# Kernel optimization log

Hardware: AMD Instinct MI355X
Metric: run time of the kernel (lower is better)

## Reference

```python
import jax, jax.numpy as jnp
import numpy as np

DIM = 768
D_STATE = 64
D_CONV = 4
EXPAND = 2
D_INNER = EXPAND * DIM          # 1536
DT_RANK = (DIM + 15) // 16      # 48
BATCH = 2
SEQ = 1024
EPS = 1e-5


def setup_inputs() -> dict:
    key = jax.random.key(0)
    ks = jax.random.split(key, 10)
    s = 0.02
    x = jax.random.normal(ks[0], (BATCH, SEQ, DIM), dtype=jnp.float32)
    gamma = jnp.ones((DIM,), jnp.float32)
    beta = jnp.zeros((DIM,), jnp.float32)
    W_in = jax.random.normal(ks[1], (2 * D_INNER, DIM), jnp.float32) * s
    conv_w = jax.random.normal(ks[2], (D_INNER, D_CONV), jnp.float32) * s
    conv_b = jnp.zeros((D_INNER,), jnp.float32)
    W_x = jax.random.normal(ks[3], (DT_RANK + 2 * D_STATE, D_INNER), jnp.float32) * s
    W_dt = jax.random.normal(ks[4], (D_INNER, DT_RANK), jnp.float32) * s
    b_dt = jax.random.uniform(ks[5], (D_INNER,), jnp.float32, -4.0, -2.0)  # dt bias ~ log-space init
    # S4D-real init: A_log[d, n] = log(n+1)
    A_log = jnp.log(jnp.broadcast_to(jnp.arange(1, D_STATE + 1, dtype=jnp.float32), (D_INNER, D_STATE)))
    D = jnp.ones((D_INNER,), jnp.float32)
    W_out = jax.random.normal(ks[6], (DIM, D_INNER), jnp.float32) * s
    return {"x": x, "gamma": gamma, "beta": beta, "W_in": W_in,
            "conv_w": conv_w, "conv_b": conv_b, "W_x": W_x,
            "W_dt": W_dt, "b_dt": b_dt, "A_log": A_log, "D": D, "W_out": W_out}


def _silu(v):
    return v * jax.nn.sigmoid(v)


def _mamba_forward(x, gamma, beta, W_in, conv_w, conv_b, W_x, W_dt, b_dt, A_log, D, W_out):
    B, L, _ = x.shape
    # LayerNorm
    mu = jnp.mean(x, axis=-1, keepdims=True)
    var = jnp.mean(jnp.square(x - mu), axis=-1, keepdims=True)
    xn = (x - mu) * jax.lax.rsqrt(var + EPS) * gamma + beta
    # in_proj -> (u, z)
    xz = jnp.einsum('bld,ed->ble', xn, W_in)          # [B, L, 2*D_INNER]
    u, z = jnp.split(xz, 2, axis=-1)                  # each [B, L, D_INNER]
    # depthwise causal conv1d along L
    uc = jnp.transpose(u, (0, 2, 1))                  # [B, C, L]
    uc = jnp.pad(uc, ((0, 0), (0, 0), (D_CONV - 1, 0)))
    kern = conv_w[:, None, :]                         # [C, 1, K]
    uc = jax.lax.conv_general_dilated(
        uc, kern, window_strides=(1,), padding='VALID',
        feature_group_count=D_INNER,
        dimension_numbers=('NCH', 'OIH', 'NCH'))
    uc = uc + conv_b[None, :, None]
    u = _silu(jnp.transpose(uc, (0, 2, 1)))           # [B, L, D_INNER]
    # x_proj -> (dt, Bssm, Cssm)
    x_dbl = jnp.einsum('blc,ec->ble', u, W_x)
    dt = x_dbl[..., :DT_RANK]
    Bssm = x_dbl[..., DT_RANK:DT_RANK + D_STATE]      # [B, L, N]
    Cssm = x_dbl[..., DT_RANK + D_STATE:]             # [B, L, N]
    delta = jax.nn.softplus(jnp.einsum('blr,cr->blc', dt, W_dt) + b_dt)  # [B, L, C]
    A = -jnp.exp(A_log)                               # [C, N]

    # selective scan, time-major
    d_t = jnp.transpose(delta, (1, 0, 2))             # [L, B, C]
    B_t = jnp.transpose(Bssm, (1, 0, 2))              # [L, B, N]
    C_t = jnp.transpose(Cssm, (1, 0, 2))              # [L, B, N]
    u_t = jnp.transpose(u, (1, 0, 2))                 # [L, B, C]

    def step(h, inp):
        d, b, c, uu = inp
        dA = jnp.exp(d[..., None] * A)                # [B, C, N]
        h = dA * h + d[..., None] * b[:, None, :] * uu[..., None]
        y = jnp.sum(h * c[:, None, :], axis=-1) + D * uu
        return h, y

    h0 = jnp.zeros((B, D_INNER, D_STATE), x.dtype)
    _, ys = jax.lax.scan(step, h0, (d_t, B_t, C_t, u_t))
    y = jnp.transpose(ys, (1, 0, 2))                  # [B, L, C]
    y = y * _silu(z)
    return jnp.einsum('blc,dc->bld', y, W_out)


def reference(x, gamma, beta, W_in, conv_w, conv_b, W_x, W_dt, b_dt, A_log, D, W_out):
    return _mamba_forward(x, gamma, beta, W_in, conv_w, conv_b, W_x,
                          W_dt, b_dt, A_log, D, W_out)
```

## Files before the change

kernel.cpp:

```cpp
#include <hip/hip_runtime.h>
#include <math.h>

#define DIMD 768
#define DSTATE 64
#define DINNER 1536
#define DTRANK 48
#define BATCH 2
#define SEQL 1024
#define NTOK (BATCH*SEQL)
#define XDBL_P 192
#define EPSV 1e-5f

typedef __attribute__((ext_vector_type(8))) short bf16x8;
typedef __attribute__((ext_vector_type(4))) float f32x4;

__device__ inline short f2bf(float f) {
  unsigned u = __float_as_uint(f);
  u = u + 0x7FFFu + ((u >> 16) & 1u);
  return (short)(u >> 16);
}

__global__ __launch_bounds__(256) void ln_kernel(const float* __restrict__ x,
                                                 const float* __restrict__ gamma,
                                                 const float* __restrict__ beta,
                                                 short* __restrict__ xnq) {
  int wave = threadIdx.x >> 6;
  int lane = threadIdx.x & 63;
  int row = blockIdx.x * 4 + wave;
  if (row >= NTOK) return;
  const float* xr = x + (size_t)row * DIMD;
  float v[12];
  float s = 0.f, ss = 0.f;
#pragma unroll
  for (int i = 0; i < 12; ++i) {
    v[i] = xr[lane + i*64];
    s += v[i];
    ss += v[i]*v[i];
  }
#pragma unroll
  for (int m = 1; m < 64; m <<= 1) {
    s  += __shfl_xor(s, m);
    ss += __shfl_xor(ss, m);
  }
  float mu   = s * (1.f/DIMD);
  float var  = ss * (1.f/DIMD) - mu*mu;
  float rstd = rsqrtf(var + EPSV);
  short* o = xnq + (size_t)row * DIMD;
#pragma unroll
  for (int i = 0; i < 12; ++i) {
    int j = lane + i*64;
    o[j] = f2bf((v[i] - mu) * rstd * gamma[j] + beta[j]);
  }
}

#define NW_IN  (3072*768)
#define NW_OUT (768*1536)
#define NW_XP  (192*1536)
__global__ __launch_bounds__(256) void cvt_weights_kernel(const float* __restrict__ Win,
                                                          const float* __restrict__ Wout,
                                                          const float* __restrict__ Wx,
                                                          short* __restrict__ qin,
                                                          short* __restrict__ qout,
                                                          short* __restrict__ qx) {
  int idx = blockIdx.x * 256 + threadIdx.x;
  if (idx < NW_IN) { qin[idx] = f2bf(Win[idx]); return; }
  idx -= NW_IN;
  if (idx < NW_OUT) { qout[idx] = f2bf(Wout[idx]); return; }
  idx -= NW_OUT;
  if (idx < NW_XP) {
    int r = idx / 1536;
    qx[idx] = (r < 176) ? f2bf(Wx[idx]) : (short)0;
  }
}

template<int BN>
__global__ __launch_bounds__(256) void gemm_mfma(const short* __restrict__ A,
                                                 const short* __restrict__ B,
                                                 float* __restrict__ C, int ldc, int K) {
  constexpr int BM = 128, BK = 64;
  constexpr int WN = (BN == 128) ? 2 : 1;
  constexpr int WM = 4 / WN;
  constexpr int MFR = BM / (WM * 16);
  constexpr int NFR = BN / (WN * 16);
  constexpr int BSW = (BN * BK * 2) / 4096;
  __shared__ short As[BM * BK];
  __shared__ short Bs[BN * BK];
  const int tid  = threadIdx.x;
  const int wave = tid >> 6, lane = tid & 63;
  const int m0 = blockIdx.y * BM;
  const int n0 = blockIdx.x * BN;
  const int wm = wave / WN, wn = wave % WN;

  const short* aSrc = A + (size_t)(m0 + (tid >> 3)) * K + (tid & 7) * 8;
  const short* bSrc = B + (size_t)(n0 + (tid >> 3)) * K + (tid & 7) * 8;

  f32x4 acc[MFR][NFR];
#pragma unroll
  for (int i = 0; i < MFR; ++i)
#pragma unroll
    for (int j = 0; j < NFR; ++j)
      acc[i][j] = (f32x4){0.f, 0.f, 0.f, 0.f};

  for (int k0 = 0; k0 < K; k0 += BK) {
#pragma unroll
    for (int s = 0; s < 4; ++s)
      __builtin_amdgcn_global_load_lds(
        (const __attribute__((address_space(1))) void*)(aSrc + (size_t)s*32*K + k0),
        (__attribute__((address_space(3))) void*)((char*)As + s*4096 + wave*1024),
        16, 0, 0);
#pragma unroll
    for (int s = 0; s < BSW; ++s)
      __builtin_amdgcn_global_load_lds(
        (const __attribute__((address_space(1))) void*)(bSrc + (size_t)s*32*K + k0),
        (__attribute__((address_space(3))) void*)((char*)Bs + s*4096 + wave*1024),
        16, 0, 0);
    __syncthreads();

#pragma unroll
    for (int kk = 0; kk < 2; ++kk) {
      bf16x8 af[MFR], bfr[NFR];
#pragma unroll
      for (int i = 0; i < MFR; ++i) {
        int r = wm * (BM / WM) + i * 16 + (lane & 15);
        af[i] = *(const bf16x8*)&As[r * BK + kk * 32 + (lane >> 4) * 8];
      }
#pragma unroll
      for (int j = 0; j < NFR; ++j) {
        int r = wn * (BN / WN) + j * 16 + (lane & 15);
        bfr[j] = *(const bf16x8*)&Bs[r * BK + kk * 32 + (lane >> 4) * 8];
      }
#pragma unroll
      for (int i = 0; i < MFR; ++i)
#pragma unroll
        for (int j = 0; j < NFR; ++j)
          acc[i][j] = __builtin_amdgcn_mfma_f32_16x16x32_bf16(af[i], bfr[j], acc[i][j], 0, 0, 0);
    }
    __syncthreads();
  }

  const int cn = lane & 15, cr4 = (lane >> 4) * 4;
#pragma unroll
  for (int i = 0; i < MFR; ++i)
#pragma unroll
    for (int j = 0; j < NFR; ++j)
#pragma unroll
      for (int r = 0; r < 4; ++r) {
        int m = m0 + wm * (BM / WM) + i * 16 + cr4 + r;
        int n = n0 + wn * (BN / WN) + j * 16 + cn;
        C[(size_t)m * ldc + n] = acc[i][j][r];
      }
}

template<int ACT>
__global__ __launch_bounds__(256) void gemm_nt(const float* __restrict__ A, int lda,
                                               const float* __restrict__ W, int ldw,
                                               const float* __restrict__ bias,
                                               float* __restrict__ C, int ldc,
                                               int M, int N, int K) {
  __shared__ float Asl[16][68];
  __shared__ float Wsl[16][68];
  int tid = threadIdx.x;
  int m0 = blockIdx.y * 64;
  int n0 = blockIdx.x * 64;
  int lrow = tid >> 2;
  int lq   = tid & 3;
  int tx = tid & 15;
  int ty = tid >> 4;
  float acc[4][4] = {{0.f}};

  for (int k0 = 0; k0 < K; k0 += 16) {
    float4 av = make_float4(0.f,0.f,0.f,0.f);
    int ar = m0 + lrow;
    if (ar < M) av = *(const float4*)(A + (size_t)ar*lda + k0 + lq*4);
    float4 wv = make_float4(0.f,0.f,0.f,0.f);
    int wr = n0 + lrow;
    if (wr < N) wv = *(const float4*)(W + (size_t)wr*ldw + k0 + lq*4);
    __syncthreads();
    Asl[lq*4+0][lrow] = av.x; Asl[lq*4+1][lrow] = av.y;
    Asl[lq*4+2][lrow] = av.z; Asl[lq*4+3][lrow] = av.w;
    Wsl[lq*4+0][lrow] = wv.x; Wsl[lq*4+1][lrow] = wv.y;
    Wsl[lq*4+2][lrow] = wv.z; Wsl[lq*4+3][lrow] = wv.w;
    __syncthreads();
#pragma unroll
    for (int kk = 0; kk < 16; ++kk) {
      float4 a4 = *(const float4*)&Asl[kk][ty*4];
      float4 w4 = *(const float4*)&Wsl[kk][tx*4];
      float a[4] = {a4.x, a4.y, a4.z, a4.w};
      float w[4] = {w4.x, w4.y, w4.z, w4.w};
#pragma unroll
      for (int i = 0; i < 4; ++i)
#pragma unroll
        for (int j = 0; j < 4; ++j)
          acc[i][j] += a[i]*w[j];
    }
  }

#pragma unroll
  for (int i = 0; i < 4; ++i) {
    int m = m0 + ty*4 + i;
    if (m >= M) continue;
    float* crow = C + (size_t)m*ldc;
    float bm = (ACT == 2) ? bias[m] : 0.f;
#pragma unroll
    for (int j = 0; j < 4; ++j) {
      int n = n0 + tx*4 + j;
      if (n >= N) continue;
      float val = acc[i][j];
      if (ACT == 2) {
        val += bm;
        val = (val > 20.f) ? val : log1pf(__expf(val));
      }
      crow[n] = val;
    }
  }
}

__global__ __launch_bounds__(256) void conv_silu_kernel(const float* __restrict__ xz,
                                                        const float* __restrict__ conv_w,
                                                        const float* __restrict__ conv_b,
                                                        float* __restrict__ uT,
                                                        short* __restrict__ ucq) {
  __shared__ float tile[64][65];
  int b  = blockIdx.z;
  int c0 = blockIdx.x * 64;
  int t0 = blockIdx.y * 64;
  int lx = threadIdx.x & 63;
  int ly = threadIdx.x >> 6;
  int c = c0 + lx;
  const int S = 2*DINNER;
  float w0 = conv_w[c*4+0], w1 = conv_w[c*4+1], w2 = conv_w[c*4+2], w3 = conv_w[c*4+3];
  float cb = conv_b[c];
#pragma unroll
  for (int i = 0; i < 16; ++i) {
    int tl = ly*16 + i;
    int t = t0 + tl;
    const float* up = xz + ((size_t)b*SEQL + t) * S + c;
    float acc = cb + up[0]*w3;
    if (t >= 1) acc += up[-1*S]*w2;
    if (t >= 2) acc += up[-2*S]*w1;
    if (t >= 3) acc += up[-3*S]*w0;
    float sig = 1.f / (1.f + __expf(-acc));
    float v = acc * sig;
    ucq[((size_t)b*SEQL + t)*DINNER + c] = f2bf(v);
    tile[lx][tl] = v;
  }
  __syncthreads();
#pragma unroll
  for (int i = 0; i < 16; ++i) {
    int cl = ly*16 + i;
    uT[((size_t)(c0 + cl))*NTOK + (size_t)b*SEQL + t0 + lx] = tile[cl][lx];
  }
}

__device__ inline float readlane_f(float v, int l) {
  return __int_as_float(__builtin_amdgcn_readlane(__float_as_int(v), l));
}

__global__ __launch_bounds__(256) void scan_kernel(const float* __restrict__ dT,
                                                   const float* __restrict__ x_dbl,
                                                   const float* __restrict__ uT,
                                                   const float* __restrict__ A_log,
                                                   const float* __restrict__ Dp,
                                                   float* __restrict__ yT) {
  __shared__ float bc[2][16*128];
  __shared__ float red_all[4][32*65 + 32];
  int tid  = threadIdx.x;
  int wave = tid >> 6;
  int lane = tid & 63;
  float* red = red_all[wave];
  int ch = blockIdx.x * 4 + wave;
  int b = ch / DINNER;
  int c = ch % DINNER;
  float Ac = -__expf(A_log[(size_t)c*64 + lane]);
  float Dc = Dp[c];
  float h = 0.f;
  const float* drow = dT + (size_t)ch * (SEQL);
  const float* dp = dT + (size_t)c * NTOK + (size_t)b * SEQL;
  const float* up = uT + (size_t)c * NTOK + (size_t)b * SEQL;
  float* yrow = yT + ((size_t)b*DINNER + c) * SEQL;
  const float* xB = x_dbl + ((size_t)b * SEQL) * XDBL_P + DTRANK;

  const int srow = tid >> 4, scol = (tid & 15) * 8;

  {
    const float* src = xB + (size_t)srow * XDBL_P + scol;
    float4 v0 = *(const float4*)(src);
    float4 v1 = *(const float4*)(src + 4);
    *(float4*)&bc[0][srow*128 + scol]     = v0;
    *(float4*)&bc[0][srow*128 + scol + 4] = v1;
  }
  float d_v = dp[lane];
  float u_v = up[lane];
  __syncthreads();

  const int NBLK = SEQL/64;
  for (int tb = 0; tb < NBLK; ++tb) {
    int t0 = tb*64;
    float d_nxt = 0.f, u_nxt = 0.f;
    if (tb + 1 < NBLK) {
      d_nxt = dp[t0 + 64 + lane];
      u_nxt = up[t0 + 64 + lane];
    }
    float du_v = d_v * u_v;

#pragma unroll
    for (int g = 0; g < 4; ++g) {
      const int cur = g & 1;
      float4 rv0, rv1;
      bool do_stage = (tb*4 + g + 1) < 64;
      if (do_stage) {
        const float* src = xB + (size_t)(t0 + (g+1)*16 + srow) * XDBL_P + scol;
        rv0 = *(const float4*)(src);
        rv1 = *(const float4*)(src + 4);
      }
      const float* bcur = &bc[cur][0];
#pragma unroll
      for (int k = 0; k < 16; ++k) {
        int i = g*16 + k;
        float sd  = readlane_f(d_v,  i);
        float sdu = readlane_f(du_v, i);
        float Bv = bcur[k*128 + lane];
        float Cv = bcur[k*128 + 64 + lane];
        float dA = __expf(sd * Ac);
        h = fmaf(dA, h, sdu * Bv);
        red[(i & 31)*65 + lane] = h * Cv;
      }
      if (g & 1) {
        int half = g >> 1;
        int r  = lane & 31;
        int hs = lane >> 5;
        float y = 0.f;
        const float* rp = &red[r*65 + hs*32];
#pragma unroll
        for (int j = 0; j < 32; ++j) y += rp[j];
        y += __shfl_xor(y, 32);
        float ut = __shfl(u_v, half*32 + r);
        y = fmaf(Dc, ut, y);
        if (lane < 32) yrow[t0 + half*32 + lane] = y;
      }
      if (do_stage) {
        *(float4*)&bc[cur^1][srow*128 + scol]     = rv0;
        *(float4*)&bc[cur^1][srow*128 + scol + 4] = rv1;
      }
      __syncthreads();
    }
    d_v = d_nxt;
    u_v = u_nxt;
  }
}

__global__ __launch_bounds__(256) void ymul_kernel(const float* __restrict__ yT,
                                                   const float* __restrict__ xz,
                                                   short* __restrict__ g) {
  __shared__ float tile[64][65];
  int b  = blockIdx.z;
  int c0 = blockIdx.x * 64;
  int t0 = blockIdx.y * 64;
  int lx = threadIdx.x & 63;
  int ly = threadIdx.x >> 6;
  const float* src = yT + ((size_t)b*DINNER + c0) * SEQL + t0;
#pragma unroll
  for (int i = 0; i < 16; ++i) {
    int c = ly*16 + i;
    tile[c][lx] = src[(size_t)c*SEQL + lx];
  }
  __syncthreads();
  const int S = 2*DINNER;
#pragma unroll
  for (int i = 0; i < 16; ++i) {
    int t = ly*16 + i;
    float z = xz[((size_t)b*SEQL + t0 + t)*S + DINNER + c0 + lx];
    float zs = z / (1.f + __expf(-z));
    g[((size_t)b*SEQL + t0 + t)*DINNER + c0 + lx] = f2bf(tile[lx][t] * zs);
  }
}

extern "C" void kernel_launch(void* const* d_in, const int* in_sizes, int n_in,
                              void* d_out, int out_size, void* d_ws, size_t ws_size,
                              hipStream_t stream) {
  const float* x      = (const float*)d_in[0];
  const float* gamma  = (const float*)d_in[1];
  const float* beta   = (const float*)d_in[2];
  const float* W_in   = (const float*)d_in[3];
  const float* conv_w = (const float*)d_in[4];
  const float* conv_b = (const float*)d_in[5];
  const float* W_x    = (const float*)d_in[6];
  const float* W_dt   = (const float*)d_in[7];
  const float* b_dt   = (const float*)d_in[8];
  const float* A_log  = (const float*)d_in[9];
  const float* Dvec   = (const float*)d_in[10];
  const float* W_out  = (const float*)d_in[11];
  float* out = (float*)d_out;

  float* ws = (float*)d_ws;
  float* xz    = ws;
  float* uT    = xz    + (size_t)NTOK*3072;
  float* xdbl  = uT    + (size_t)NTOK*1536;
  float* dltT  = xdbl  + (size_t)NTOK*XDBL_P;
  float* yT    = dltT  + (size_t)NTOK*1536;
  short* xnq   = (short*)(yT + (size_t)NTOK*1536);
  short* ucq   = xnq  + (size_t)NTOK*768;
  short* gq    = ucq  + (size_t)NTOK*1536;
  short* qin   = gq   + (size_t)NTOK*1536;
  short* qx    = qin  + (size_t)NW_IN;
  short* qout  = qx   + (size_t)NW_XP;

  cvt_weights_kernel<<<(NW_IN+NW_OUT+NW_XP+255)/256, 256, 0, stream>>>(W_in, W_out, W_x, qin, qout, qx);
  ln_kernel<<<NTOK/4, 256, 0, stream>>>(x, gamma, beta, xnq);
  gemm_mfma<128><<<dim3(3072/128, NTOK/128), 256, 0, stream>>>(xnq, qin, xz, 3072, DIMD);
  conv_silu_kernel<<<dim3(DINNER/64, SEQL/64, BATCH), 256, 0, stream>>>(xz, conv_w, conv_b, uT, ucq);
  gemm_mfma<64><<<dim3(XDBL_P/64, NTOK/128), 256, 0, stream>>>(ucq, qx, xdbl, XDBL_P, DINNER);
  gemm_nt<2><<<dim3(NTOK/64, DINNER/64), 256, 0, stream>>>(W_dt, DTRANK, xdbl, XDBL_P, b_dt,
                                                           dltT, NTOK, DINNER, NTOK, DTRANK);
  scan_kernel<<<BATCH*DINNER/4, 256, 0, stream>>>(dltT, xdbl, uT, A_log, Dvec, yT);
  ymul_kernel<<<dim3(DINNER/64, SEQL/64, BATCH), 256, 0, stream>>>(yT, xz, gq);
  gemm_mfma<64><<<dim3(DIMD/64, NTOK/128), 256, 0, stream>>>(gq, qout, out, DIMD, DINNER);
}
```

Before: 214.7 us.

## Split-K the x_proj GEMM and reduce scan partial sums every 16 steps

The x_proj GEMM (N=192, only 3x16 blocks) now runs with a 4-way split over K into partial buffers, followed by a separate reduction kernel, so that more blocks are available to fill the GPU. The scan kernel reduces its h*C products every 16 timesteps instead of 32, which halves the reduction scratch in LDS and spreads the reduction work more evenly. It also switches from __expf to exp2f with a pre-scaled A. The split-K path adds extra global traffic for the partials and one more kernel launch.

```diff
diff --git a/kernel.cpp b/kernel.cpp
--- a/kernel.cpp
+++ b/kernel.cpp
@@ -76,7 +76,8 @@
 template<int BN>
 __global__ __launch_bounds__(256) void gemm_mfma(const short* __restrict__ A,
                                                  const short* __restrict__ B,
-                                                 float* __restrict__ C, int ldc, int K) {
+                                                 float* __restrict__ C, int ldc,
+                                                 int Kfull, int Kchunk, size_t partStride) {
   constexpr int BM = 128, BK = 64;
   constexpr int WN = (BN == 128) ? 2 : 1;
   constexpr int WM = 4 / WN;
@@ -90,9 +91,12 @@
   const int m0 = blockIdx.y * BM;
   const int n0 = blockIdx.x * BN;
   const int wm = wave / WN, wn = wave % WN;
-
-  const short* aSrc = A + (size_t)(m0 + (tid >> 3)) * K + (tid & 7) * 8;
-  const short* bSrc = B + (size_t)(n0 + (tid >> 3)) * K + (tid & 7) * 8;
+  const int kBeg = blockIdx.z * Kchunk;
+  const int kEnd = kBeg + Kchunk;
+  C += (size_t)blockIdx.z * partStride;
+
+  const short* aSrc = A + (size_t)(m0 + (tid >> 3)) * Kfull + (tid & 7) * 8;
+  const short* bSrc = B + (size_t)(n0 + (tid >> 3)) * Kfull + (tid & 7) * 8;
 
   f32x4 acc[MFR][NFR];
 #pragma unroll
@@ -101,17 +105,17 @@
     for (int j = 0; j < NFR; ++j)
       acc[i][j] = (f32x4){0.f, 0.f, 0.f, 0.f};
 
-  for (int k0 = 0; k0 < K; k0 += BK) {
+  for (int k0 = kBeg; k0 < kEnd; k0 += BK) {
 #pragma unroll
     for (int s = 0; s < 4; ++s)
       __builtin_amdgcn_global_load_lds(
-        (const __attribute__((address_space(1))) void*)(aSrc + (size_t)s*32*K + k0),
+        (const __attribute__((address_space(1))) void*)(aSrc + (size_t)s*32*Kfull + k0),
         (__attribute__((address_space(3))) void*)((char*)As + s*4096 + wave*1024),
         16, 0, 0);
 #pragma unroll
     for (int s = 0; s < BSW; ++s)
       __builtin_amdgcn_global_load_lds(
-        (const __attribute__((address_space(1))) void*)(bSrc + (size_t)s*32*K + k0),
+        (const __attribute__((address_space(1))) void*)(bSrc + (size_t)s*32*Kfull + k0),
         (__attribute__((address_space(3))) void*)((char*)Bs + s*4096 + wave*1024),
         16, 0, 0);
     __syncthreads();
@@ -149,6 +153,24 @@
         int n = n0 + wn * (BN / WN) + j * 16 + cn;
         C[(size_t)m * ldc + n] = acc[i][j][r];
       }
+}
+
+__global__ __launch_bounds__(256) void reduce4_kernel(const float* __restrict__ p,
+                                                      float* __restrict__ outb) {
+  const int n4 = NTOK * XDBL_P / 4;
+  int i = blockIdx.x * 256 + threadIdx.x;
+  if (i >= n4) return;
+  const float4* p4 = (const float4*)p;
+  float4 a = p4[i];
+  float4 b = p4[i + n4];
+  float4 c = p4[i + 2*n4];
+  float4 d = p4[i + 3*n4];
+  float4 r;
+  r.x = ((a.x + b.x) + c.x) + d.x;
+  r.y = ((a.y + b.y) + c.y) + d.y;
+  r.z = ((a.z + b.z) + c.z) + d.z;
+  r.w = ((a.w + b.w) + c.w) + d.w;
+  ((float4*)outb)[i] = r;
 }
 
 template<int ACT>
@@ -263,7 +285,7 @@
                                                    const float* __restrict__ Dp,
                                                    float* __restrict__ yT) {
   __shared__ float bc[2][16*128];
-  __shared__ float red_all[4][32*65 + 32];
+  __shared__ float red_all[4][16*65 + 16];
   int tid  = threadIdx.x;
   int wave = tid >> 6;
   int lane = tid & 63;
@@ -271,28 +293,25 @@
   int ch = blockIdx.x * 4 + wave;
   int b = ch / DINNER;
   int c = ch % DINNER;
-  float Ac = -__expf(A_log[(size_t)c*64 + lane]);
+  float Ac2 = -__expf(A_log[(size_t)c*64 + lane]) * 1.44269504f;
   float Dc = Dp[c];
   float h = 0.f;
-  const float* drow = dT + (size_t)ch * (SEQL);
   const float* dp = dT + (size_t)c * NTOK + (size_t)b * SEQL;
   const float* up = uT + (size_t)c * NTOK + (size_t)b * SEQL;
   float* yrow = yT + ((size_t)b*DINNER + c) * SEQL;
   const float* xB = x_dbl + ((size_t)b * SEQL) * XDBL_P + DTRANK;
 
   const int srow = tid >> 4, scol = (tid & 15) * 8;
-
   {
     const float* src = xB + (size_t)srow * XDBL_P + scol;
-    float4 v0 = *(const float4*)(src);
-    float4 v1 = *(const float4*)(src + 4);
-    *(float4*)&bc[0][srow*128 + scol]     = v0;
-    *(float4*)&bc[0][srow*128 + scol + 4] = v1;
+    *(float4*)&bc[0][srow*128 + scol]     = *(const float4*)(src);
+    *(float4*)&bc[0][srow*128 + scol + 4] = *(const float4*)(src + 4);
   }
   float d_v = dp[lane];
   float u_v = up[lane];
   __syncthreads();
 
+  const int r = lane & 15, hs = lane >> 4;
   const int NBLK = SEQL/64;
   for (int tb = 0; tb < NBLK; ++tb) {
     int t0 = tb*64;
@@ -321,22 +340,20 @@
         float sdu = readlane_f(du_v, i);
         float Bv = bcur[k*128 + lane];
         float Cv = bcur[k*128 + 64 + lane];
-        float dA = __expf(sd * Ac);
+        float dA = exp2f(sd * Ac2);
         h = fmaf(dA, h, sdu * Bv);
-        red[(i & 31)*65 + lane] = h * Cv;
-      }
-      if (g & 1) {
-        int half = g >> 1;
-        int r  = lane & 31;
-        int hs = lane >> 5;
+        red[k*65 + lane] = h * Cv;
+      }
+      {
         float y = 0.f;
-        const float* rp = &red[r*65 + hs*32];
-#pragma unroll
-        for (int j = 0; j < 32; ++j) y += rp[j];
+        const float* rp = &red[r*65 + hs*16];
+#pragma unroll
+        for (int j = 0; j < 16; ++j) y += rp[j];
+        y += __shfl_xor(y, 16);
         y += __shfl_xor(y, 32);
-        float ut = __shfl(u_v, half*32 + r);
+        float ut = __shfl(u_v, g*16 + r);
         y = fmaf(Dc, ut, y);
-        if (lane < 32) yrow[t0 + half*32 + lane] = y;
+        if (lane < 16) yrow[t0 + g*16 + lane] = y;
       }
       if (do_stage) {
         *(float4*)&bc[cur^1][srow*128 + scol]     = rv0;
@@ -398,7 +415,8 @@
   float* xdbl  = uT    + (size_t)NTOK*1536;
   float* dltT  = xdbl  + (size_t)NTOK*XDBL_P;
   float* yT    = dltT  + (size_t)NTOK*1536;
-  short* xnq   = (short*)(yT + (size_t)NTOK*1536);
+  float* xpart = yT    + (size_t)NTOK*1536;
+  short* xnq   = (short*)(xpart + (size_t)4*NTOK*XDBL_P);
   short* ucq   = xnq  + (size_t)NTOK*768;
   short* gq    = ucq  + (size_t)NTOK*1536;
   short* qin   = gq   + (size_t)NTOK*1536;
@@ -407,12 +425,15 @@
 
   cvt_weights_kernel<<<(NW_IN+NW_OUT+NW_XP+255)/256, 256, 0, stream>>>(W_in, W_out, W_x, qin, qout, qx);
   ln_kernel<<<NTOK/4, 256, 0, stream>>>(x, gamma, beta, xnq);
-  gemm_mfma<128><<<dim3(3072/128, NTOK/128), 256, 0, stream>>>(xnq, qin, xz, 3072, DIMD);
+  gemm_mfma<128><<<dim3(3072/128, NTOK/128), 256, 0, stream>>>(xnq, qin, xz, 3072, DIMD, DIMD, 0);
   conv_silu_kernel<<<dim3(DINNER/64, SEQL/64, BATCH), 256, 0, stream>>>(xz, conv_w, conv_b, uT, ucq);
-  gemm_mfma<64><<<dim3(XDBL_P/64, NTOK/128), 256, 0, stream>>>(ucq, qx, xdbl, XDBL_P, DINNER);
+  gemm_mfma<64><<<dim3(XDBL_P/64, NTOK/128, 4), 256, 0, stream>>>(ucq, qx, xpart, XDBL_P,
+                                                                  DINNER, DINNER/4,
+                                                                  (size_t)NTOK*XDBL_P);
+  reduce4_kernel<<<(NTOK*XDBL_P/4 + 255)/256, 256, 0, stream>>>(xpart, xdbl);
   gemm_nt<2><<<dim3(NTOK/64, DINNER/64), 256, 0, stream>>>(W_dt, DTRANK, xdbl, XDBL_P, b_dt,
                                                            dltT, NTOK, DINNER, NTOK, DTRANK);
   scan_kernel<<<BATCH*DINNER/4, 256, 0, stream>>>(dltT, xdbl, uT, A_log, Dvec, yT);
   ymul_kernel<<<dim3(DINNER/64, SEQL/64, BATCH), 256, 0, stream>>>(yT, xz, gq);
-  gemm_mfma<64><<<dim3(DIMD/64, NTOK/128), 256, 0, stream>>>(gq, qout, out, DIMD, DINNER);
-}
+  gemm_mfma<64><<<dim3(DIMD/64, NTOK/128), 256, 0, stream>>>(gq, qout, out, DIMD, DINNER, DINNER, 0);
+}
```

After: 222.6 us. +3.7%, slower.
